# Optimization experiments

Hardware: AMD Instinct MI355X
Metric: run time of the kernel (lower is better)

The kernel has to match this reference:

```python
import jax, jax.numpy as jnp
import numpy as np

N_DIMS = 8
N_REGIMES = 8
CAPACITY = 16
KERNEL = 2
DILATIONS = (1, 2, 4, 8)
BOTTLE = (32, 32, 32, 32)
B = 128
T_LEN = 512
N_STEPS = T_LEN - CAPACITY


def setup_inputs() -> dict:
    key = jax.random.key(0)
    ks = jax.random.split(key, 8)
    x = jax.random.normal(ks[0], (B, N_DIMS, T_LEN), jnp.float32)
    temp = jnp.ones((), jnp.float32)
    u = jax.random.uniform(ks[1], (N_STEPS, B, 1, N_REGIMES), jnp.float32)

    def mkw(k, o, i):
        return jax.random.normal(k, (o, i, KERNEL), jnp.float32) / np.float32(np.sqrt(i * KERNEL))

    c_in = N_DIMS + N_REGIMES
    w0 = mkw(ks[2], BOTTLE[0], c_in)
    b0 = jnp.zeros((BOTTLE[0],), jnp.float32)
    w1 = mkw(ks[3], BOTTLE[1], BOTTLE[0])
    b1 = jnp.zeros((BOTTLE[1],), jnp.float32)
    w2 = mkw(ks[4], BOTTLE[2], BOTTLE[1])
    b2 = jnp.zeros((BOTTLE[2],), jnp.float32)
    w3 = mkw(ks[5], N_REGIMES, BOTTLE[3])
    b3 = jnp.zeros((N_REGIMES,), jnp.float32)
    return {"x": x, "temp": temp, "u": u, "w0": w0, "b0": b0, "w1": w1,
            "b1": b1, "w2": w2, "b2": b2, "w3": w3, "b3": b3, "T": T_LEN}


def _conv(h, w, b, d):
    # causal dilated conv1d, VALID padding (windowing handles causality)
    out = jax.lax.conv_general_dilated(h, w, (1,), 'VALID', rhs_dilation=(d,),
                                       dimension_numbers=('NCH', 'OIH', 'NCH'))
    return out + b[None, :, None]


def _forward(x, temp, u, params, T):
    cap = CAPACITY
    pad = sum(DILATIONS)  # F.pad(x, (sum(dilations), 0)) -> left-pad time axis
    xpad = jnp.pad(x, ((0, 0), (0, 0), (pad, 0)))
    n_steps = T - cap
    # windows x_pad[:, :, t-cap:t] for t in [cap, T) -> (n_steps, B, D, cap)
    idx = jnp.arange(n_steps)[:, None] + jnp.arange(cap)[None, :]
    xw = jnp.transpose(xpad[:, :, idx], (2, 0, 1, 3))
    g = -jnp.log(-jnp.log(u + 1e-10) + 1e-10)  # Gumbel(0,1) noise
    Bn = x.shape[0]
    K = u.shape[-1]
    z0 = jnp.zeros((Bn, K, cap), x.dtype)  # capacity initial zero regimes
    layers = tuple(zip(params[0::2], params[1::2], DILATIONS))

    def step(zbuf, inp):
        xw_t, g_t = inp  # (B, D, cap), (B, 1, K)
        h = jnp.concatenate([xw_t, zbuf], axis=1)  # (B, D+K, cap)
        for (w, b, d) in layers:
            h = jax.nn.elu(_conv(h, w, b, d))
        logq = jax.nn.log_softmax(h[:, :, -1], axis=1)  # (B, K)
        y = jax.nn.softmax((logq + g_t[:, 0, :]) / temp, axis=-1)  # gumbel-softmax sample
        zbuf = jnp.concatenate([zbuf[:, :, 1:], y[:, :, None]], axis=2)
        return zbuf, (y, logq)

    _, (zs, logqs) = jax.lax.scan(step, z0, (xw, g))
    z_all = jnp.concatenate([z0, jnp.transpose(zs, (1, 2, 0))], axis=2)  # (B, K, T)
    logq_out = jnp.transpose(logqs, (1, 2, 0))[..., None]  # (B, K, n_steps, 1) = torch.stack(dim=2)
    return z_all, logq_out


def reference(x, temp, u, w0, b0, w1, b1, w2, b2, w3, b3, T):
    return _forward(x, temp, u, (w0, b0, w1, b1, w2, b2, w3, b3), T)
```

## Files before the change

### kernel.cpp

```cpp
#include <hip/hip_runtime.h>

#define NB      128
#define ND      8
#define NK      8
#define TLEN    512
#define NSTEPS  496

#define INVLN2f 1.44269504088896340736f

__device__ __forceinline__ float fexp(float x) { return __expf(x); }
__device__ __forceinline__ float flog(float x) { return __logf(x); }
__device__ __forceinline__ float frcp(float x) { return __builtin_amdgcn_rcpf(x); }
__device__ __forceinline__ float elur(float x) { return x > 0.f ? x : fexp(x) - 1.f; }

#if defined(__has_builtin)
#if __has_builtin(__builtin_amdgcn_exp2f)
#define fexp2(x) __builtin_amdgcn_exp2f(x)
#endif
#endif
#ifndef fexp2
#define fexp2(x) exp2f(x)
#endif

#define DPP_QP0(v)  __int_as_float(__builtin_amdgcn_mov_dpp(__float_as_int(v), 0x00, 0xF, 0xF, false))
#define DPP_QP1(v)  __int_as_float(__builtin_amdgcn_mov_dpp(__float_as_int(v), 0x55, 0xF, 0xF, false))
#define DPP_QP2(v)  __int_as_float(__builtin_amdgcn_mov_dpp(__float_as_int(v), 0xAA, 0xF, 0xF, false))
#define DPP_QP3(v)  __int_as_float(__builtin_amdgcn_mov_dpp(__float_as_int(v), 0xFF, 0xF, 0xF, false))
#define DPP_ROR4(v) __int_as_float(__builtin_amdgcn_mov_dpp(__float_as_int(v), 0x124, 0xF, 0xF, false))
#define DPP_X1(v)   __int_as_float(__builtin_amdgcn_mov_dpp(__float_as_int(v), 0xB1, 0xF, 0xF, false))
#define DPP_X2(v)   __int_as_float(__builtin_amdgcn_mov_dpp(__float_as_int(v), 0x4E, 0xF, 0xF, false))

#define RED8_MAX(m) { m = fmaxf(m, DPP_X1(m)); m = fmaxf(m, DPP_X2(m)); m = fmaxf(m, DPP_ROR4(m)); }
#define RED8_SUM(s) { s = s + DPP_X1(s); s = s + DPP_X2(s); s = s + DPP_ROR4(s); }

#if defined(__has_builtin)
#if __has_builtin(__builtin_amdgcn_permlane32_swap)
#define HAVE_PLSWAP 1
#endif
#endif
#ifdef HAVE_PLSWAP
typedef unsigned int uint2v __attribute__((ext_vector_type(2)));
__device__ __forceinline__ float xhalfsum(float v) {
    unsigned int u = __float_as_uint(v);
    uint2v r = __builtin_amdgcn_permlane32_swap(u, u, false, false);
    return __uint_as_float(r[0]) + __uint_as_float(r[1]);
}
#else
__device__ __forceinline__ float xhalfsum(float v) { return v + __shfl_xor(v, 32); }
#endif

__device__ __forceinline__ void ldot16x2(const float* p, const float* wn, const float* wo,
                                         float& dn, float& dd) {
    const float4* q4 = (const float4*)p;
    float n0 = 0.f, n1 = 0.f, o0 = 0.f, o1 = 0.f;
    #pragma unroll
    for (int i = 0; i < 4; ++i) {
        float4 v = q4[i];
        n0 = fmaf(wn[4*i+0], v.x, n0);
        n1 = fmaf(wn[4*i+1], v.y, n1);
        o0 = fmaf(wo[4*i+0], v.x, o0);
        o1 = fmaf(wo[4*i+1], v.y, o1);
        n0 = fmaf(wn[4*i+2], v.z, n0);
        n1 = fmaf(wn[4*i+3], v.w, n1);
        o0 = fmaf(wo[4*i+2], v.z, o0);
        o1 = fmaf(wo[4*i+3], v.w, o1);
    }
    dn = n0 + n1;
    dd = o0 + o1;
}

#define STEP(qv, S1, S2, S3, ZP, ZC, RP, RC, DO_OUT)                              \
  {                                                                               \
    const int q_ = (qv);                                                          \
            \
    float g2_own = 0.f;                                                           \
    if (DO_OUT) g2_own = gls[(q_ - 15) * NK + o3];                                \
    const float4* _xq = (const float4*)&xcol[q_ + tap][0];                        \
    float4 _xa = _xq[0], _xb = _xq[1];                                            \
               \
    float _z0 = fmaf(wzn[0], ZC[0], 0.f);                                         \
    float _z1 = fmaf(wzn[1], ZC[1], 0.f);                                         \
    float _z2 = fmaf(wzn[2], ZC[2], 0.f);                                         \
    float _z3 = fmaf(wzn[3], ZC[3], 0.f);                                         \
    _z0 = fmaf(wzn[4], ZC[4], _z0);                                               \
    _z1 = fmaf(wzn[5], ZC[5], _z1);                                               \
    _z2 = fmaf(wzn[6], ZC[6], _z2);                                               \
    _z3 = fmaf(wzn[7], ZC[7], _z3);                                               \
    float o0v = elur(fmaf((_z0 + _z1) + (_z2 + _z3), RC, XZ));                    \
    bc0[lane] = o0v;                                                              \
                                                                     \
    float n1, d1o;                                                                \
    ldot16x2(bc0 + hoff, w1n, w1o, n1, d1o);                                      \
    float o1v = elur(xhalfsum(n1) + P1[S1]);                                      \
    bc1[lane] = o1v;                                                              \
    P1[S1] = b1r + xhalfsum(d1o);                                                 \
                                                                     \
    float n2, d2o;                                                                \
    ldot16x2(bc1 + hoff, w2n, w2o, n2, d2o);                                      \
    float o2v = elur(xhalfsum(n2) + P2[S2]);                                      \
    bc2[lane] = o2v;                                                              \
    P2[S2] = b2r + xhalfsum(d2o);                                                 \
                                                                     \
    float n3, d3o;                                                                \
    ldot16x2(bc2 + hoff, w3n, w3o, n3, d3o);                                      \
    float a3m = elur(xhalfsum(n3) + P3[S3]);                                      \
    P3[S3] = b3r + xhalfsum(d3o);                                                 \
    if (DO_OUT) {                                                                 \
                            \
      float F = fexp2(fmaf(a3m, klog, g2_own));                                   \
      float S = F; RED8_SUM(S);                                                   \
      float r2 = frcp(S);                                                         \
      RP = r2;                                                                    \
      float _t = DPP_ROR4(F);                                                     \
      ZP[0] = DPP_QP0(F);  ZP[1] = DPP_QP1(F);  ZP[2] = DPP_QP2(F);               \
      ZP[3] = DPP_QP3(F);                                                         \
      ZP[4] = DPP_QP0(_t); ZP[5] = DPP_QP1(_t); ZP[6] = DPP_QP2(_t);              \
      ZP[7] = DPP_QP3(_t);                                                        \
                   \
      {                                                                           \
        float z0 = fmaf(wzo[0], ZP[0], fmaf(wzo[1], ZP[1], 0.f));                 \
        float z1 = fmaf(wzo[2], ZP[2], fmaf(wzo[3], ZP[3], 0.f));                 \
        float z2 = fmaf(wzo[4], ZP[4], fmaf(wzo[5], ZP[5], 0.f));                 \
        float z3 = fmaf(wzo[6], ZP[6], fmaf(wzo[7], ZP[7], 0.f));                 \
        ZQ2n = ((z0 + z1) + (z2 + z3)) * r2;                                      \
      }                                                                           \
                      \
      float mx = a3m; RED8_MAX(mx);                                               \
      float e = fexp(a3m - mx);                                                   \
      float se = e; RED8_SUM(se);                                                 \
      float lse = mx + flog(se);                                                  \
      if (lane < 8) {                                                             \
        outg[zoff + lane * TLEN + q_ + 1]       = F * r2;                         \
        outg[qoff + lane * NSTEPS + (q_ - 15)]  = a3m - lse;                      \
      }                                                                           \
    }                                                                             \
       \
    {                                                                             \
      float s0 = fmaf(wxr[0], _xa.x, fmaf(wxr[1], _xa.y, 0.f));                   \
      float s1 = fmaf(wxr[2], _xa.z, fmaf(wxr[3], _xa.w, 0.f));                   \
      float s2 = fmaf(wxr[4], _xb.x, fmaf(wxr[5], _xb.y, 0.f));                   \
      float s3 = fmaf(wxr[6], _xb.z, fmaf(wxr[7], _xb.w, 0.f));                   \
      float xp = (s0 + s1) + (s2 + s3);                                           \
      XZ = xhalfsum(xp) + b0r + ZQ2;                                              \
      ZQ2 = ZQ2n;                                                                 \
    }                                                                             \
  }

__global__ __launch_bounds__(64, 1)
void regime_scan_kernel(const float* __restrict__ xg,
                        const float* __restrict__ tempg,
                        const float* __restrict__ ug,
                        const float* __restrict__ w0g,
                        const float* __restrict__ b0g,
                        const float* __restrict__ w1g,
                        const float* __restrict__ b1g,
                        const float* __restrict__ w2g,
                        const float* __restrict__ b2g,
                        const float* __restrict__ w3g,
                        const float* __restrict__ b3g,
                        float* __restrict__ outg)
{
    __shared__ __align__(16) float xcol[527][8];
    __shared__ __align__(16) float gls[NSTEPS * NK];
    __shared__ __align__(16) float bc0[64], bc1[64], bc2[64];

    const int lane = threadIdx.x;
    const int b    = blockIdx.x;
    const int c    = lane & 31;
    const int o3   = lane & 7;
    const int half = lane >> 5;
    const int hoff = half << 4;
    const int tap  = (lane < 32) ? 1 : 0;
    const int p4   = (lane & 4);

    float wzn[8], wzo[8];
    #pragma unroll
    for (int k = 0; k < 8; ++k) {
        int ch = k ^ p4;
        wzn[k] = w0g[c * 32 + (8 + ch) * 2 + 1];
        wzo[k] = w0g[c * 32 + (8 + ch) * 2 + 0];
    }
    float wxr[8];
    #pragma unroll
    for (int d = 0; d < 8; ++d) wxr[d] = w0g[c * 32 + d * 2 + tap];
    float w1n[16], w1o[16], w2n[16], w2o[16], w3n[16], w3o[16];
    #pragma unroll
    for (int i = 0; i < 16; ++i) {
        int j = hoff + i;
        w1n[i] = w1g[c * 64 + j * 2 + 1];
        w1o[i] = w1g[c * 64 + j * 2 + 0];
        w2n[i] = w2g[c * 64 + j * 2 + 1];
        w2o[i] = w2g[c * 64 + j * 2 + 0];
        w3n[i] = w3g[o3 * 64 + j * 2 + 1];
        w3o[i] = w3g[o3 * 64 + j * 2 + 0];
    }
    const float b0r  = b0g[c];
    const float b1r  = b1g[c];
    const float b2r  = b2g[c];
    const float b3r  = b3g[o3];
    const float tinv = frcp(tempg[0]);
    const float klog = tinv * INVLN2f;

    if (lane < 15) {
        #pragma unroll
        for (int d = 0; d < ND; ++d) xcol[lane][d] = 0.f;
    }
    const float* xb = xg + b * (ND * TLEN);
    for (int t = lane; t < TLEN; t += 64) {
        #pragma unroll
        for (int d = 0; d < ND; ++d) xcol[15 + t][d] = xb[d * TLEN + t];
    }
    for (int idx = lane; idx < NSTEPS * NK; idx += 64) {
        int s = idx >> 3, k = idx & 7;
        float uu = ug[s * (NB * NK) + b * NK + k];
        float g  = -flog(-flog(uu + 1e-10f) + 1e-10f);
        gls[idx] = g * klog;
    }
    const int zoff = b * (NK * TLEN);
    const int qoff = NB * NK * TLEN + b * (NK * NSTEPS);
    for (int idx = lane; idx < NK * 16; idx += 64) {
        outg[zoff + (idx >> 4) * TLEN + (idx & 15)] = 0.f;
    }

    float zA[8], zB[8];
    #pragma unroll
    for (int k = 0; k < 8; ++k) { zA[k] = 0.f; zB[k] = 0.f; }
    float RA = 1.f, RB = 1.f;
    float P1[2] = { b1r, b1r };
    float P2[4] = { b2r, b2r, b2r, b2r };
    float P3[8];
    #pragma unroll
    for (int k = 0; k < 8; ++k) P3[k] = b3r;
    float ZQ2 = 0.f, ZQ2n = 0.f;
    float XZ;
    {
        const float4* xq = (const float4*)&xcol[tap][0];
        float4 xa = xq[0], xbv = xq[1];
        float s0 = fmaf(wxr[0], xa.x, fmaf(wxr[1], xa.y, 0.f));
        float s1 = fmaf(wxr[2], xa.z, fmaf(wxr[3], xa.w, 0.f));
        float s2 = fmaf(wxr[4], xbv.x, fmaf(wxr[5], xbv.y, 0.f));
        float s3 = fmaf(wxr[6], xbv.z, fmaf(wxr[7], xbv.w, 0.f));
        XZ = xhalfsum((s0 + s1) + (s2 + s3)) + b0r;
    }

    #pragma unroll
    for (int q = 1; q <= 14; ++q) STEP(q, q & 1, q & 3, q & 7, zA, zB, RA, RB, 0);

    for (int qb = 15; qb <= 503; qb += 8) {
        #pragma unroll
        for (int u = 0; u < 8; u += 2) {
            STEP(qb + u,     (15 + u) & 1, (15 + u) & 3, (15 + u) & 7, zA, zB, RA, RB, 1);
            STEP(qb + u + 1, (16 + u) & 1, (16 + u) & 3, (16 + u) & 7, zB, zA, RB, RA, 1);
        }
    }
}

extern "C" void kernel_launch(void* const* d_in, const int* in_sizes, int n_in,
                              void* d_out, int out_size, void* d_ws, size_t ws_size,
                              hipStream_t stream) {
    (void)in_sizes; (void)n_in; (void)out_size; (void)d_ws; (void)ws_size;
    regime_scan_kernel<<<dim3(NB), dim3(64), 0, stream>>>(
        (const float*)d_in[0],
        (const float*)d_in[1],
        (const float*)d_in[2],
        (const float*)d_in[3],
        (const float*)d_in[4],
        (const float*)d_in[5],
        (const float*)d_in[6],
        (const float*)d_in[7],
        (const float*)d_in[8],
        (const float*)d_in[9],
        (const float*)d_in[10],
        (float*)d_out);
}
```

Measured before the change: 364.1 us.

## Replace LDS broadcast dot products with DPP row rotations and permlane swaps

```diff
diff --git a/kernel.cpp b/kernel.cpp
--- a/kernel.cpp
+++ b/kernel.cpp
@@ -29,17 +29,23 @@
 #define DPP_ROR4(v) __int_as_float(__builtin_amdgcn_mov_dpp(__float_as_int(v), 0x124, 0xF, 0xF, false))
 #define DPP_X1(v)   __int_as_float(__builtin_amdgcn_mov_dpp(__float_as_int(v), 0xB1, 0xF, 0xF, false))
 #define DPP_X2(v)   __int_as_float(__builtin_amdgcn_mov_dpp(__float_as_int(v), 0x4E, 0xF, 0xF, false))
+#define DPP_RORN(v, ctrl) __int_as_float(__builtin_amdgcn_mov_dpp(__float_as_int(v), (ctrl), 0xF, 0xF, false))
 
 #define RED8_MAX(m) { m = fmaxf(m, DPP_X1(m)); m = fmaxf(m, DPP_X2(m)); m = fmaxf(m, DPP_ROR4(m)); }
 #define RED8_SUM(s) { s = s + DPP_X1(s); s = s + DPP_X2(s); s = s + DPP_ROR4(s); }
 
 #if defined(__has_builtin)
 #if __has_builtin(__builtin_amdgcn_permlane32_swap)
-#define HAVE_PLSWAP 1
-#endif
-#endif
-#ifdef HAVE_PLSWAP
+#define HAVE_PLSWAP32 1
+#endif
+#if __has_builtin(__builtin_amdgcn_permlane16_swap)
+#define HAVE_PLSWAP16 1
+#endif
+#endif
+
 typedef unsigned int uint2v __attribute__((ext_vector_type(2)));
+
+#ifdef HAVE_PLSWAP32
 __device__ __forceinline__ float xhalfsum(float v) {
     unsigned int u = __float_as_uint(v);
     uint2v r = __builtin_amdgcn_permlane32_swap(u, u, false, false);
@@ -49,35 +55,47 @@
 __device__ __forceinline__ float xhalfsum(float v) { return v + __shfl_xor(v, 32); }
 #endif
 
-__device__ __forceinline__ void ldot16x2(const float* p, const float* wn, const float* wo,
-                                         float& dn, float& dd) {
-    const float4* q4 = (const float4*)p;
-    float n0 = 0.f, n1 = 0.f, o0 = 0.f, o1 = 0.f;
-    #pragma unroll
-    for (int i = 0; i < 4; ++i) {
-        float4 v = q4[i];
-        n0 = fmaf(wn[4*i+0], v.x, n0);
-        n1 = fmaf(wn[4*i+1], v.y, n1);
-        o0 = fmaf(wo[4*i+0], v.x, o0);
-        o1 = fmaf(wo[4*i+1], v.y, o1);
-        n0 = fmaf(wn[4*i+2], v.z, n0);
-        n1 = fmaf(wn[4*i+3], v.w, n1);
-        o0 = fmaf(wo[4*i+2], v.z, o0);
-        o1 = fmaf(wo[4*i+3], v.w, o1);
-    }
-    dn = n0 + n1;
-    dd = o0 + o1;
-}
+#ifdef HAVE_PLSWAP16
+#define PLSWAP16(dst, v) { \
+    unsigned int _u = __float_as_uint(v); \
+    uint2v _pr = __builtin_amdgcn_permlane16_swap(_u, _u, false, false); \
+    dst = __uint_as_float(sel16 ? _pr[0] : _pr[1]); }
+#else
+#define PLSWAP16(dst, v) { dst = __shfl_xor((v), 16); }
+#endif
+
+#define ROTF(r, na, oa, WN, WO) { \
+    float _v = DPP_RORN(_bs, 0x120 + (r)); \
+    na = fmaf(WN[r], _v, na); \
+    oa = fmaf(WO[r], _v, oa); }
+
+#define GATHER_DOT(ov, WN, WO, nres, ores)                                        \
+  {                                                                               \
+    float _swp;                                                                   \
+    PLSWAP16(_swp, ov);                                                           \
+    float _bs = useown ? (ov) : _swp;                                             \
+    float _n0 = WN[0] * _bs, _oA = WO[0] * _bs;                                   \
+    float _n1 = 0.f, _oB = 0.f, _n2 = 0.f, _oC = 0.f, _n3 = 0.f, _oD = 0.f;       \
+    ROTF(1,  _n1, _oB, WN, WO) ROTF(2,  _n2, _oC, WN, WO)                         \
+    ROTF(3,  _n3, _oD, WN, WO) ROTF(4,  _n0, _oA, WN, WO)                         \
+    ROTF(5,  _n1, _oB, WN, WO) ROTF(6,  _n2, _oC, WN, WO)                         \
+    ROTF(7,  _n3, _oD, WN, WO) ROTF(8,  _n0, _oA, WN, WO)                         \
+    ROTF(9,  _n1, _oB, WN, WO) ROTF(10, _n2, _oC, WN, WO)                         \
+    ROTF(11, _n3, _oD, WN, WO) ROTF(12, _n0, _oA, WN, WO)                         \
+    ROTF(13, _n1, _oB, WN, WO) ROTF(14, _n2, _oC, WN, WO)                         \
+    ROTF(15, _n3, _oD, WN, WO)                                                    \
+    nres = (_n0 + _n1) + (_n2 + _n3);                                             \
+    ores = (_oA + _oB) + (_oC + _oD);                                             \
+  }
 
 #define STEP(qv, S1, S2, S3, ZP, ZC, RP, RC, DO_OUT)                              \
   {                                                                               \
     const int q_ = (qv);                                                          \
-            \
     float g2_own = 0.f;                                                           \
     if (DO_OUT) g2_own = gls[(q_ - 15) * NK + o3];                                \
     const float4* _xq = (const float4*)&xcol[q_ + tap][0];                        \
     float4 _xa = _xq[0], _xb = _xq[1];                                            \
-               \
+                                                                     \
     float _z0 = fmaf(wzn[0], ZC[0], 0.f);                                         \
     float _z1 = fmaf(wzn[1], ZC[1], 0.f);                                         \
     float _z2 = fmaf(wzn[2], ZC[2], 0.f);                                         \
@@ -87,22 +105,19 @@
     _z2 = fmaf(wzn[6], ZC[6], _z2);                                               \
     _z3 = fmaf(wzn[7], ZC[7], _z3);                                               \
     float o0v = elur(fmaf((_z0 + _z1) + (_z2 + _z3), RC, XZ));                    \
-    bc0[lane] = o0v;                                                              \
-                                                                     \
+                                                   \
     float n1, d1o;                                                                \
-    ldot16x2(bc0 + hoff, w1n, w1o, n1, d1o);                                      \
+    GATHER_DOT(o0v, w1n, w1o, n1, d1o);                                           \
     float o1v = elur(xhalfsum(n1) + P1[S1]);                                      \
-    bc1[lane] = o1v;                                                              \
     P1[S1] = b1r + xhalfsum(d1o);                                                 \
                                                                      \
     float n2, d2o;                                                                \
-    ldot16x2(bc1 + hoff, w2n, w2o, n2, d2o);                                      \
+    GATHER_DOT(o1v, w2n, w2o, n2, d2o);                                           \
     float o2v = elur(xhalfsum(n2) + P2[S2]);                                      \
-    bc2[lane] = o2v;                                                              \
     P2[S2] = b2r + xhalfsum(d2o);                                                 \
                                                                      \
     float n3, d3o;                                                                \
-    ldot16x2(bc2 + hoff, w3n, w3o, n3, d3o);                                      \
+    GATHER_DOT(o2v, w3n, w3o, n3, d3o);                                           \
     float a3m = elur(xhalfsum(n3) + P3[S3]);                                      \
     P3[S3] = b3r + xhalfsum(d3o);                                                 \
     if (DO_OUT) {                                                                 \
@@ -124,7 +139,7 @@
         float z3 = fmaf(wzo[6], ZP[6], fmaf(wzo[7], ZP[7], 0.f));                 \
         ZQ2n = ((z0 + z1) + (z2 + z3)) * r2;                                      \
       }                                                                           \
-                      \
+                                                \
       float mx = a3m; RED8_MAX(mx);                                               \
       float e = fexp(a3m - mx);                                                   \
       float se = e; RED8_SUM(se);                                                 \
@@ -134,7 +149,7 @@
         outg[qoff + lane * NSTEPS + (q_ - 15)]  = a3m - lse;                      \
       }                                                                           \
     }                                                                             \
-       \
+                                           \
     {                                                                             \
       float s0 = fmaf(wxr[0], _xa.x, fmaf(wxr[1], _xa.y, 0.f));                   \
       float s1 = fmaf(wxr[2], _xa.z, fmaf(wxr[3], _xa.w, 0.f));                   \
@@ -162,16 +177,30 @@
 {
     __shared__ __align__(16) float xcol[527][8];
     __shared__ __align__(16) float gls[NSTEPS * NK];
-    __shared__ __align__(16) float bc0[64], bc1[64], bc2[64];
 
     const int lane = threadIdx.x;
     const int b    = blockIdx.x;
     const int c    = lane & 31;
     const int o3   = lane & 7;
-    const int half = lane >> 5;
-    const int hoff = half << 4;
+    const int l15  = lane & 15;
+    const int hbase = (lane >> 5) << 4;
     const int tap  = (lane < 32) ? 1 : 0;
     const int p4   = (lane & 4);
+    const int myrow = lane >> 4;
+    const bool useown = (myrow == 0) || (myrow == 3);
+
+    int dir;
+    {
+        int rr1 = __builtin_amdgcn_mov_dpp(l15, 0x121, 0xF, 0xF, false);
+        dir = (rr1 == ((l15 + 1) & 15)) ? 1 : -1;
+    }
+    bool sel16 = false;
+#ifdef HAVE_PLSWAP16
+    {
+        uint2v pr = __builtin_amdgcn_permlane16_swap((unsigned)lane, (unsigned)lane, false, false);
+        sel16 = (pr[0] == (unsigned)(lane ^ 16));
+    }
+#endif
 
     float wzn[8], wzo[8];
     #pragma unroll
@@ -185,14 +214,14 @@
     for (int d = 0; d < 8; ++d) wxr[d] = w0g[c * 32 + d * 2 + tap];
     float w1n[16], w1o[16], w2n[16], w2o[16], w3n[16], w3o[16];
     #pragma unroll
-    for (int i = 0; i < 16; ++i) {
-        int j = hoff + i;
-        w1n[i] = w1g[c * 64 + j * 2 + 1];
-        w1o[i] = w1g[c * 64 + j * 2 + 0];
-        w2n[i] = w2g[c * 64 + j * 2 + 1];
-        w2o[i] = w2g[c * 64 + j * 2 + 0];
-        w3n[i] = w3g[o3 * 64 + j * 2 + 1];
-        w3o[i] = w3g[o3 * 64 + j * 2 + 0];
+    for (int r = 0; r < 16; ++r) {
+        int j = hbase + ((l15 + dir * r) & 15);
+        w1n[r] = w1g[c * 64 + j * 2 + 1];
+        w1o[r] = w1g[c * 64 + j * 2 + 0];
+        w2n[r] = w2g[c * 64 + j * 2 + 1];
+        w2o[r] = w2g[c * 64 + j * 2 + 0];
+        w3n[r] = w3g[o3 * 64 + j * 2 + 1];
+        w3o[r] = w3g[o3 * 64 + j * 2 + 0];
     }
     const float b0r  = b0g[c];
     const float b1r  = b1g[c];
@@ -221,6 +250,7 @@
     for (int idx = lane; idx < NK * 16; idx += 64) {
         outg[zoff + (idx >> 4) * TLEN + (idx & 15)] = 0.f;
     }
+    __syncthreads();
 
     float zA[8], zB[8];
     #pragma unroll
```

New measurement: 390.2 us. 7.2% more time.
